# Kernel optimization log

Measured on AMD Instinct MI355X. Metric: run time of the kernel, lower is better.

The kernel has to match this reference:

```python
import jax, jax.numpy as jnp
import numpy as np

EPSILON = 0.5

def setup_inputs() -> dict:
    key = jax.random.key(0)
    k1, k2, k3 = jax.random.split(key, 3)
    N, F, D = 8192, 128, 64
    X = jax.random.normal(k1, (N, F), dtype=jnp.float32)
    W_r = jax.random.normal(k2, (2 * F, D), dtype=jnp.float32)
    a_r = jax.random.normal(k3, (D,), dtype=jnp.float32)
    return {"X": X, "W_r": W_r, "a_r": a_r}

def reference(X, W_r, a_r):
    # Faithful to: cat(X_i, X_j) @ W_r @ a_r == (X @ W1 @ a_r)[i] + (X @ W2 @ a_r)[j]
    # (standard GAT decomposition -- avoids materializing [N, N, 2F]).
    F_ = X.shape[1]
    w1 = W_r[:F_] @ a_r          # [F]
    w2 = W_r[F_:] @ a_r          # [F]
    s1 = X @ w1                  # [N]
    s2 = X @ w2                  # [N]
    R = jax.nn.leaky_relu(s1[:, None] + s2[None, :])   # [N, N]
    # torch .std() is unbiased (ddof=1) over all elements
    R = (R - R.mean()) / (jnp.std(R, ddof=1) + 1e-5)
    E = jax.nn.softmax(R, axis=1)
    threshold = E.mean() / EPSILON
    filtered_E = jnp.where(E >= threshold, jnp.float32(1.0), jnp.float32(0.0))
    return filtered_E
```

## Files before the change

### kernel.cpp

```cpp
#include <hip/hip_runtime.h>
#include <math.h>

#define Nn 8192

static constexpr int S1o = 256;
static constexpr int S2o = S1o + Nn;
static constexpr int Mo  = S2o + Nn;
static constexpr int Zo  = Mo + Nn;
static constexpr int RRo = Zo + Nn;
static constexpr int STo = RRo + Nn;

typedef float nfloat4 __attribute__((ext_vector_type(4)));

__device__ __forceinline__ float lrelu32(float z) {
    return (z >= 0.0f) ? z : __fmul_rn(0.01f, z);
}

__device__ __forceinline__ double exp_fast(double x) {
    x = fmin(fmax(x, -700.0), 700.0);
    const double INVLN2 = 1.44269504088896338700e+00;
    const double LN2HI  = 6.93147180369123816490e-01;
    const double LN2LO  = 1.90821492927058770002e-10;
    double nd = rint(x * INVLN2);
    double r  = fma(-nd, LN2HI, x);
    r = fma(-nd, LN2LO, r);
    double p = 1.56192069685862264622e-10;
    p = fma(p, r, 2.08767569878680989792e-09);
    p = fma(p, r, 2.50521083854417187751e-08);
    p = fma(p, r, 2.75573192239858906526e-07);
    p = fma(p, r, 2.75573192239858925110e-06);
    p = fma(p, r, 2.48015873015873015873e-05);
    p = fma(p, r, 1.98412698412698412698e-04);
    p = fma(p, r, 1.38888888888888894069e-03);
    p = fma(p, r, 8.33333333333333321769e-03);
    p = fma(p, r, 4.16666666666666643537e-02);
    p = fma(p, r, 1.66666666666666657415e-01);
    p = fma(p, r, 5.00000000000000000000e-01);
    p = fma(p, r, 1.0);
    p = fma(p, r, 1.0);
    long long n = (long long)nd;
    double sc = __longlong_as_double((n + 1023LL) << 52);
    return p * sc;
}
__device__ __forceinline__ float exp32cr(float x) {
    return (float)exp_fast((double)x);
}

__device__ float blas_dot(const float* __restrict__ a, const float* __restrict__ x, int n) {
    float lane[8];
#pragma unroll
    for (int l = 0; l < 8; ++l) lane[l] = 0.0f;
    for (int k = 0; k < n; k += 8) {
#pragma unroll
        for (int l = 0; l < 8; ++l) lane[l] = __fmaf_rn(a[k + l], x[k + l], lane[l]);
    }
    float s0 = __fadd_rn(lane[0], lane[4]);
    float s1 = __fadd_rn(lane[1], lane[5]);
    float s2 = __fadd_rn(lane[2], lane[6]);
    float s3 = __fadd_rn(lane[3], lane[7]);
    return __fadd_rn(__fadd_rn(s0, s1), __fadd_rn(s2, s3));
}

__device__ __forceinline__ unsigned f2key(float f) {
    unsigned u = __float_as_uint(f);
    return (u & 0x80000000u) ? ~u : (u | 0x80000000u);
}
__device__ __forceinline__ float key2f(unsigned k) {
    unsigned u = (k & 0x80000000u) ? (k & 0x7FFFFFFFu) : ~k;
    return __uint_as_float(u);
}

#define ROW_REDUCE_TAIL(RESULT_STMT)                                          \
    {                                                                         \
        __syncthreads();                                                      \
        if (t < 64) {                                                         \
            float sl = __fadd_rn(__fadd_rn(red[t * 8 + 0], red[t * 8 + 1]),   \
                                 __fadd_rn(red[t * 8 + 2], red[t * 8 + 3]));  \
            float sr = __fadd_rn(__fadd_rn(red[t * 8 + 4], red[t * 8 + 5]),   \
                                 __fadd_rn(red[t * 8 + 6], red[t * 8 + 7]));  \
            LA[t] = __fadd_rn(sl, sr);                                        \
        }                                                                     \
        __syncthreads();                                                      \
        {                                                                     \
            float* src = LA;                                                  \
            float* dst = LB;                                                  \
            for (int s = 32; s >= 1; s >>= 1) {                               \
                if (t < s) dst[t] = __fadd_rn(src[2 * t], src[2 * t + 1]);    \
                __syncthreads();                                              \
                float* tmp = src; src = dst; dst = tmp;                       \
            }                                                                 \
            if (t == 0) { RESULT_STMT; }                                      \
        }                                                                     \
    }

__global__ __launch_bounds__(256) void k_s(const float* __restrict__ X,
                                           const float* __restrict__ Wr,
                                           const float* __restrict__ ar,
                                           float* __restrict__ scr) {
    __shared__ float w1[128], w2[128];
    int t = threadIdx.x;
    if (t < 128) {
        w1[t] = blas_dot(Wr + t * 64, ar, 64);
        w2[t] = blas_dot(Wr + (128 + t) * 64, ar, 64);
    }
    __syncthreads();
    int i = blockIdx.x * 256 + t;
    scr[S1o + i] = blas_dot(X + i * 128, w1, 128);
    scr[S2o + i] = blas_dot(X + i * 128, w2, 128);
}

template <int MODE>
__global__ __launch_bounds__(512) void k_rows_stat8(const float* __restrict__ scr,
                                                    float* __restrict__ rowred) {
    __shared__ float red[512];
    __shared__ float LA[64], LB[32];
    int r0 = blockIdx.x * 8, t = threadIdx.x;
    int l = t >> 3, c = t & 7;
    const float* s2 = scr + S2o;
    int ebase = l * 128 + c;
    float sv[16];
#pragma unroll
    for (int k = 0; k < 16; ++k) sv[k] = s2[ebase + 8 * k];
    float mu = (MODE == 1) ? scr[STo] : 0.0f;
    for (int rr = 0; rr < 8; ++rr) {
        float s1i = scr[S1o + r0 + rr];
        float r;
        if (MODE == 0) {
            r = lrelu32(__fadd_rn(s1i, sv[0]));
#pragma unroll
            for (int k = 1; k < 16; ++k)
                r = __fadd_rn(r, lrelu32(__fadd_rn(s1i, sv[k])));
        } else {
            float d0 = __fsub_rn(lrelu32(__fadd_rn(s1i, sv[0])), mu);
            r = __fmul_rn(d0, d0);
#pragma unroll
            for (int k = 1; k < 16; ++k) {
                float d = __fsub_rn(lrelu32(__fadd_rn(s1i, sv[k])), mu);
                r = __fadd_rn(r, __fmul_rn(d, d));
            }
        }
        red[t] = r;
        ROW_REDUCE_TAIL(rowred[r0 + rr] = src[0])
    }
}

template <int MODE>
__global__ __launch_bounds__(1024) void k_tree(const float* __restrict__ rowred,
                                               float* __restrict__ scr) {
    __shared__ float A[8192];
    __shared__ float B[4096];
    int t = threadIdx.x;
    for (int idx = t; idx < 8192; idx += 1024) A[idx] = rowred[idx];
    __syncthreads();
    float* src = A;
    float* dst = B;
    for (int s = 4096; s >= 1; s >>= 1) {
        for (int idx = t; idx < s; idx += 1024)
            dst[idx] = __fadd_rn(src[2 * idx], src[2 * idx + 1]);
        __syncthreads();
        float* tmp = src; src = dst; dst = tmp;
    }
    if (t == 0) {
        float total = src[0];
        if (MODE == 0) {
            scr[STo] = __fdiv_rn(total, 67108864.0f);
        } else if (MODE == 1) {
            float var = __fdiv_rn(total, 67108864.0f);
            scr[STo + 1] = __fadd_rn(__fsqrt_rn(var), 1e-5f);
        } else {
            float mean = __fdiv_rn(total, 67108864.0f);
            scr[STo + 2] = __fdiv_rn(mean, 0.5f);
        }
    }
}

__global__ __launch_bounds__(512) void k_MZE(float* __restrict__ scr,
                                             float* __restrict__ rowred) {
    __shared__ float red[512];
    __shared__ float LA[64], LB[32];
    __shared__ float Zsh;
    int i = blockIdx.x, t = threadIdx.x;
    int l = t >> 3, c = t & 7;
    const float* s2 = scr + S2o;
    float s1i = scr[S1o + i];
    float mu = scr[STo], sig = scr[STo + 1];
    int ebase = l * 128 + c;

    float rn[16];
    float mx = -3.4e38f;
#pragma unroll
    for (int k = 0; k < 16; ++k) {
        float Rn = __fdiv_rn(__fsub_rn(lrelu32(__fadd_rn(s1i, s2[ebase + 8 * k])), mu), sig);
        rn[k] = Rn;
        mx = fmaxf(mx, Rn);
    }
    red[t] = mx;
    __syncthreads();
    for (int s = 256; s >= 1; s >>= 1) {
        if (t < s) red[t] = fmaxf(red[t], red[t + s]);
        __syncthreads();
    }
    float Mi = red[0];
    __syncthreads();

    float p[16];
    p[0] = exp32cr(__fsub_rn(rn[0], Mi));
    float r = p[0];
#pragma unroll
    for (int k = 1; k < 16; ++k) {
        p[k] = exp32cr(__fsub_rn(rn[k], Mi));
        r = __fadd_rn(r, p[k]);
    }
    red[t] = r;
    ROW_REDUCE_TAIL(Zsh = src[0]; scr[Zo + i] = src[0]; scr[Mo + i] = Mi)
    __syncthreads();
    float Zi = Zsh;

    float e = __fdiv_rn(p[0], Zi);
#pragma unroll
    for (int k = 1; k < 16; ++k)
        e = __fadd_rn(e, __fdiv_rn(p[k], Zi));
    red[t] = e;
    ROW_REDUCE_TAIL(rowred[i] = src[0])
}

__global__ __launch_bounds__(256) void k_cut(float* __restrict__ scr) {
    int i = blockIdx.x * 256 + threadIdx.x;
    if (i >= Nn) return;
    float s1i = scr[S1o + i];
    float mu = scr[STo], sig = scr[STo + 1], thr = scr[STo + 2];
    float Mi = scr[Mo + i], Zi = scr[Zo + i];
    double thr_d = (double)thr;
    unsigned lo[3] = {0x00800000u, 0x00800000u, 0x00800000u};
    unsigned hi[3] = {0xFF800000u, 0xFF800000u, 0xFF800000u};
    for (int it = 0; it < 32; ++it) {
        unsigned mid[3];
        double m[3];
#pragma unroll
        for (int w = 0; w < 3; ++w) {
            mid[w] = lo[w] + ((hi[w] - lo[w]) >> 1);
            float s2v = key2f(mid[w]);
            float Rn = __fdiv_rn(__fsub_rn(lrelu32(__fadd_rn(s1i, s2v)), mu), sig);
            float P = exp32cr(__fsub_rn(Rn, Mi));
            float E = __fdiv_rn(P, Zi);
            m[w] = ((double)E - thr_d) / thr_d;
        }
        bool p0 = (m[0] >= -2.8e-8);
        bool p1 = (m[1] > 2.8e-8);
        bool p2 = (m[2] >= 1.75e-7);
        if (p0) hi[0] = mid[0]; else lo[0] = mid[0] + 1;
        if (p1) hi[1] = mid[1]; else lo[1] = mid[1] + 1;
        if (p2) hi[2] = mid[2]; else lo[2] = mid[2] + 1;
    }
    scr[Mo + i]  = __uint_as_float(lo[0]);
    scr[Zo + i]  = __uint_as_float(lo[1]);
    scr[RRo + i] = __uint_as_float(lo[2]);
}

__global__ __launch_bounds__(256) void k_out(const float* __restrict__ scr,
                                             float* __restrict__ out) {
    int t = threadIdx.x;
    int r0 = blockIdx.x * 8;
    const float* s2 = scr + S2o;
    unsigned kA[8], kB[8], kC[8];
    long long rowbase[8];
#pragma unroll
    for (int rr = 0; rr < 8; ++rr) {
        int i = r0 + rr;
        kA[rr] = __float_as_uint(scr[Mo + i]);
        kB[rr] = __float_as_uint(scr[Zo + i]);
        kC[rr] = __float_as_uint(scr[RRo + i]);
        rowbase[rr] = (long long)i * Nn;
    }
    for (int ch = 0; ch < 8; ++ch) {
        int j0 = ch * 1024 + t * 4;
        nfloat4 sv = *reinterpret_cast<const nfloat4*>(s2 + j0);
        unsigned k0 = f2key(sv.x), k1 = f2key(sv.y), k2 = f2key(sv.z), k3 = f2key(sv.w);
#pragma unroll
        for (int rr = 0; rr < 8; ++rr) {
            unsigned a = kA[rr], b = kB[rr], cc = kC[rr];
            nfloat4 r;
            r.x = (k0 < a) ? 0.0f : (k0 < b) ? 1.0f : (k0 < cc) ? 0.0f : 1.0f;
            r.y = (k1 < a) ? 0.0f : (k1 < b) ? 1.0f : (k1 < cc) ? 0.0f : 1.0f;
            r.z = (k2 < a) ? 0.0f : (k2 < b) ? 1.0f : (k2 < cc) ? 0.0f : 1.0f;
            r.w = (k3 < a) ? 0.0f : (k3 < b) ? 1.0f : (k3 < cc) ? 0.0f : 1.0f;
            __builtin_nontemporal_store(r, reinterpret_cast<nfloat4*>(out + rowbase[rr] + j0));
        }
    }
}

extern "C" void kernel_launch(void* const* d_in, const int* in_sizes, int n_in,
                              void* d_out, int out_size, void* d_ws, size_t ws_size,
                              hipStream_t stream) {
    const float *X = nullptr, *Wr = nullptr, *ar = nullptr;
    for (int k = 0; k < n_in; ++k) {
        if      (in_sizes[k] == 1048576) X  = (const float*)d_in[k];
        else if (in_sizes[k] == 16384)   Wr = (const float*)d_in[k];
        else if (in_sizes[k] == 64)      ar = (const float*)d_in[k];
    }
    if (!X)  X  = (const float*)d_in[0];
    if (!Wr) Wr = (const float*)d_in[1];
    if (!ar) ar = (const float*)d_in[2];

    float* out = (float*)d_out;
    float* scr = (float*)d_ws;
    float* rowred = scr + RRo;

    k_s            <<<32,   256, 0, stream>>>(X, Wr, ar, scr);
    k_rows_stat8<0><<<1024, 512, 0, stream>>>(scr, rowred);
    k_tree<0>      <<<1,   1024, 0, stream>>>(rowred, scr);
    k_rows_stat8<1><<<1024, 512, 0, stream>>>(scr, rowred);
    k_tree<1>      <<<1,   1024, 0, stream>>>(rowred, scr);
    k_MZE          <<<Nn,   512, 0, stream>>>(scr, rowred);
    k_tree<2>      <<<1,   1024, 0, stream>>>(rowred, scr);
    k_cut          <<<32,   256, 0, stream>>>(scr);
    k_out          <<<1024, 256, 0, stream>>>(scr, out);
}
```

Measured before the change: 215.1 us.

## Use wavefront shuffles for row reductions and fold threshold search into output kernel

Row reductions now use wavefront shuffle trees instead of repeated shared-memory passes with a __syncthreads per level. The max reduction in k_MZE uses xor shuffles plus a small per-wave array. The separate k_cut kernel is removed. Each k_out block runs its own 24 binary searches in parallel threads, one per row and bound, and the searches now stop early. This saves a launch and spreads the serial search work across many blocks, but the rest of each k_out block waits at a barrier while those threads search.

```diff
diff --git a/kernel.cpp b/kernel.cpp
--- a/kernel.cpp
+++ b/kernel.cpp
@@ -70,7 +70,7 @@
     return __uint_as_float(u);
 }
 
-#define ROW_REDUCE_TAIL(RESULT_STMT)                                          \
+#define ROW_REDUCE_TAIL_SHFL(RESULT_STMT)                                     \
     {                                                                         \
         __syncthreads();                                                      \
         if (t < 64) {                                                         \
@@ -78,19 +78,15 @@
                                  __fadd_rn(red[t * 8 + 2], red[t * 8 + 3]));  \
             float sr = __fadd_rn(__fadd_rn(red[t * 8 + 4], red[t * 8 + 5]),   \
                                  __fadd_rn(red[t * 8 + 6], red[t * 8 + 7]));  \
-            LA[t] = __fadd_rn(sl, sr);                                        \
+            float v = __fadd_rn(sl, sr);                                      \
+            _Pragma("unroll") for (int s_ = 32; s_ >= 1; s_ >>= 1) {          \
+                float a_ = __shfl(v, (2 * t) & 63);                           \
+                float b_ = __shfl(v, (2 * t + 1) & 63);                       \
+                if (t < s_) v = __fadd_rn(a_, b_);                            \
+            }                                                                 \
+            if (t == 0) { float total = v; RESULT_STMT; }                     \
         }                                                                     \
         __syncthreads();                                                      \
-        {                                                                     \
-            float* src = LA;                                                  \
-            float* dst = LB;                                                  \
-            for (int s = 32; s >= 1; s >>= 1) {                               \
-                if (t < s) dst[t] = __fadd_rn(src[2 * t], src[2 * t + 1]);    \
-                __syncthreads();                                              \
-                float* tmp = src; src = dst; dst = tmp;                       \
-            }                                                                 \
-            if (t == 0) { RESULT_STMT; }                                      \
-        }                                                                     \
     }
 
 __global__ __launch_bounds__(256) void k_s(const float* __restrict__ X,
@@ -113,7 +109,6 @@
 __global__ __launch_bounds__(512) void k_rows_stat8(const float* __restrict__ scr,
                                                     float* __restrict__ rowred) {
     __shared__ float red[512];
-    __shared__ float LA[64], LB[32];
     int r0 = blockIdx.x * 8, t = threadIdx.x;
     int l = t >> 3, c = t & 7;
     const float* s2 = scr + S2o;
@@ -140,7 +135,7 @@
             }
         }
         red[t] = r;
-        ROW_REDUCE_TAIL(rowred[r0 + rr] = src[0])
+        ROW_REDUCE_TAIL_SHFL(rowred[r0 + rr] = total)
     }
 }
 
@@ -177,7 +172,7 @@
 __global__ __launch_bounds__(512) void k_MZE(float* __restrict__ scr,
                                              float* __restrict__ rowred) {
     __shared__ float red[512];
-    __shared__ float LA[64], LB[32];
+    __shared__ float wmax[8];
     __shared__ float Zsh;
     int i = blockIdx.x, t = threadIdx.x;
     int l = t >> 3, c = t & 7;
@@ -194,14 +189,12 @@
         rn[k] = Rn;
         mx = fmaxf(mx, Rn);
     }
-    red[t] = mx;
+#pragma unroll
+    for (int o = 32; o > 0; o >>= 1) mx = fmaxf(mx, __shfl_xor(mx, o));
+    if ((t & 63) == 0) wmax[t >> 6] = mx;
     __syncthreads();
-    for (int s = 256; s >= 1; s >>= 1) {
-        if (t < s) red[t] = fmaxf(red[t], red[t + s]);
-        __syncthreads();
-    }
-    float Mi = red[0];
-    __syncthreads();
+    float Mi = fmaxf(fmaxf(fmaxf(wmax[0], wmax[1]), fmaxf(wmax[2], wmax[3])),
+                     fmaxf(fmaxf(wmax[4], wmax[5]), fmaxf(wmax[6], wmax[7])));
 
     float p[16];
     p[0] = exp32cr(__fsub_rn(rn[0], Mi));
@@ -212,8 +205,7 @@
         r = __fadd_rn(r, p[k]);
     }
     red[t] = r;
-    ROW_REDUCE_TAIL(Zsh = src[0]; scr[Zo + i] = src[0]; scr[Mo + i] = Mi)
-    __syncthreads();
+    ROW_REDUCE_TAIL_SHFL(Zsh = total; scr[Zo + i] = total; scr[Mo + i] = Mi)
     float Zi = Zsh;
 
     float e = __fdiv_rn(p[0], Zi);
@@ -221,57 +213,48 @@
     for (int k = 1; k < 16; ++k)
         e = __fadd_rn(e, __fdiv_rn(p[k], Zi));
     red[t] = e;
-    ROW_REDUCE_TAIL(rowred[i] = src[0])
-}
-
-__global__ __launch_bounds__(256) void k_cut(float* __restrict__ scr) {
-    int i = blockIdx.x * 256 + threadIdx.x;
-    if (i >= Nn) return;
-    float s1i = scr[S1o + i];
+    ROW_REDUCE_TAIL_SHFL(rowred[i] = total)
+}
+
+__global__ __launch_bounds__(256) void k_out(const float* __restrict__ scr,
+                                             float* __restrict__ out) {
+    __shared__ unsigned kcut[8][3];
+    int t = threadIdx.x;
+    int r0 = blockIdx.x * 8;
     float mu = scr[STo], sig = scr[STo + 1], thr = scr[STo + 2];
-    float Mi = scr[Mo + i], Zi = scr[Zo + i];
-    double thr_d = (double)thr;
-    unsigned lo[3] = {0x00800000u, 0x00800000u, 0x00800000u};
-    unsigned hi[3] = {0xFF800000u, 0xFF800000u, 0xFF800000u};
-    for (int it = 0; it < 32; ++it) {
-        unsigned mid[3];
-        double m[3];
-#pragma unroll
-        for (int w = 0; w < 3; ++w) {
-            mid[w] = lo[w] + ((hi[w] - lo[w]) >> 1);
-            float s2v = key2f(mid[w]);
+    if (t < 24) {
+        int rr = t / 3, w = t - rr * 3;
+        int i = r0 + rr;
+        float s1i = scr[S1o + i];
+        float Mi = scr[Mo + i], Zi = scr[Zo + i];
+        double thr_d = (double)thr;
+        unsigned lo = 0x00800000u;
+        unsigned hi = 0xFF800000u;
+        while (lo < hi) {
+            unsigned mid = lo + ((hi - lo) >> 1);
+            float s2v = key2f(mid);
             float Rn = __fdiv_rn(__fsub_rn(lrelu32(__fadd_rn(s1i, s2v)), mu), sig);
             float P = exp32cr(__fsub_rn(Rn, Mi));
             float E = __fdiv_rn(P, Zi);
-            m[w] = ((double)E - thr_d) / thr_d;
+            double m = ((double)E - thr_d) / thr_d;
+            bool pred = (w == 0) ? (m >= -2.8e-8)
+                      : (w == 1) ? (m > 2.8e-8)
+                                 : (m >= 1.75e-7);
+            if (pred) hi = mid; else lo = mid + 1;
         }
-        bool p0 = (m[0] >= -2.8e-8);
-        bool p1 = (m[1] > 2.8e-8);
-        bool p2 = (m[2] >= 1.75e-7);
-        if (p0) hi[0] = mid[0]; else lo[0] = mid[0] + 1;
-        if (p1) hi[1] = mid[1]; else lo[1] = mid[1] + 1;
-        if (p2) hi[2] = mid[2]; else lo[2] = mid[2] + 1;
-    }
-    scr[Mo + i]  = __uint_as_float(lo[0]);
-    scr[Zo + i]  = __uint_as_float(lo[1]);
-    scr[RRo + i] = __uint_as_float(lo[2]);
-}
-
-__global__ __launch_bounds__(256) void k_out(const float* __restrict__ scr,
-                                             float* __restrict__ out) {
-    int t = threadIdx.x;
-    int r0 = blockIdx.x * 8;
-    const float* s2 = scr + S2o;
+        kcut[rr][w] = lo;
+    }
+    __syncthreads();
     unsigned kA[8], kB[8], kC[8];
     long long rowbase[8];
 #pragma unroll
     for (int rr = 0; rr < 8; ++rr) {
-        int i = r0 + rr;
-        kA[rr] = __float_as_uint(scr[Mo + i]);
-        kB[rr] = __float_as_uint(scr[Zo + i]);
-        kC[rr] = __float_as_uint(scr[RRo + i]);
-        rowbase[rr] = (long long)i * Nn;
-    }
+        kA[rr] = kcut[rr][0];
+        kB[rr] = kcut[rr][1];
+        kC[rr] = kcut[rr][2];
+        rowbase[rr] = (long long)(r0 + rr) * Nn;
+    }
+    const float* s2 = scr + S2o;
     for (int ch = 0; ch < 8; ++ch) {
         int j0 = ch * 1024 + t * 4;
         nfloat4 sv = *reinterpret_cast<const nfloat4*>(s2 + j0);
@@ -313,6 +296,5 @@
     k_tree<1>      <<<1,   1024, 0, stream>>>(rowred, scr);
     k_MZE          <<<Nn,   512, 0, stream>>>(scr, rowred);
     k_tree<2>      <<<1,   1024, 0, stream>>>(rowred, scr);
-    k_cut          <<<32,   256, 0, stream>>>(scr);
     k_out          <<<1024, 256, 0, stream>>>(scr, out);
 }
```

Measured after the change: 210.8 us. 1.02x faster.
